# Kernel optimization log

Measured on AMD Instinct MI355X. Metric: run time of the kernel, lower is better.

## Reference

```python
import jax, jax.numpy as jnp
import numpy as np

B, CIN, COUT, H0 = 2, 256, 256, 128
GN_G = 16

def hsig(x):
    return jnp.clip(x + 3.0, 0.0, 6.0) / 6.0

def conv3x3(x, w, b):
    y = jax.lax.conv_general_dilated(x, w, (1, 1), ((1, 1), (1, 1)),
                                     dimension_numbers=('NCHW', 'OIHW', 'NCHW'))
    return y + b[None, :, None, None]

def group_norm(x, gamma, beta):
    Bn, C, H, W = x.shape
    xr = x.reshape(Bn, GN_G, C // GN_G, H, W)
    m = xr.mean((2, 3, 4), keepdims=True)
    v = xr.var((2, 3, 4), keepdims=True)
    xn = ((xr - m) * jax.lax.rsqrt(v + 1e-5)).reshape(Bn, C, H, W)
    return xn * gamma[None, :, None, None] + beta[None, :, None, None]

def mdconv(x, offset, mask, weight, stride):
    # Modulated deformable conv v2, 3x3 kernel, padding=1, zero-pad bilinear sampling.
    Bn, C, H, W = x.shape
    K2 = mask.shape[1]  # 9 kernel taps
    Ho, Wo = mask.shape[2], mask.shape[3]
    off = offset.reshape(Bn, K2, 2, Ho, Wo)  # (dy, dx) per tap (mmcv channel order)
    ki = jnp.arange(K2)
    py = (jnp.arange(Ho, dtype=x.dtype) * stride - 1.0)[None, None, :, None] \
         + (ki // 3).astype(x.dtype)[None, :, None, None] + off[:, :, 0]
    px = (jnp.arange(Wo, dtype=x.dtype) * stride - 1.0)[None, None, None, :] \
         + (ki % 3).astype(x.dtype)[None, :, None, None] + off[:, :, 1]
    y0f = jnp.floor(py); x0f = jnp.floor(px)
    wy = py - y0f; wx = px - x0f
    y0 = y0f.astype(jnp.int32); x0 = x0f.astype(jnp.int32)
    xf = x.reshape(Bn, C, H * W)

    def gather(yy, xx):
        valid = ((yy >= 0) & (yy < H) & (xx >= 0) & (xx < W)).astype(x.dtype)
        idx = jnp.clip(yy, 0, H - 1) * W + jnp.clip(xx, 0, W - 1)
        g = jax.vmap(lambda f, i: f[:, i])(xf, idx.reshape(Bn, -1))
        return g.reshape(Bn, C, K2, Ho, Wo) * valid[:, None]

    val = (gather(y0, x0) * ((1 - wy) * (1 - wx))[:, None]
           + gather(y0, x0 + 1) * ((1 - wy) * wx)[:, None]
           + gather(y0 + 1, x0) * (wy * (1 - wx))[:, None]
           + gather(y0 + 1, x0 + 1) * (wy * wx)[:, None])
    val = val * mask[:, None]
    return jnp.einsum('bckhw,ock->bohw', val, weight.reshape(weight.shape[0], C, K2))

def scale_attn(f, w, b):
    p = f.mean((2, 3))                  # global avg pool -> (B, C)
    s = hsig(jax.nn.relu(p @ w.T + b))  # (B, 1)
    return s[:, :, None, None]

def dyrelu(x, w1, b1, w2, b2):
    Bn, C = x.shape[0], x.shape[1]
    p = x.mean((2, 3))
    h = jax.nn.relu(p @ w1.T + b1)
    c = (hsig(h @ w2.T + b2) - 0.5).reshape(Bn, 4, C)  # a1, b1, a2, b2
    e = lambda t: t[:, :, None, None]
    a1 = c[:, 0] * 2.0 + 1.0
    a2 = c[:, 2] * 2.0
    return jnp.maximum(x * e(a1) + e(c[:, 1]), x * e(a2) + e(c[:, 3]))

def resize_align(x, Ho, Wo):
    # bilinear resize, align_corners=True
    Bn, C, H, W = x.shape
    sy = jnp.arange(Ho, dtype=x.dtype) * ((H - 1) / (Ho - 1))
    sx = jnp.arange(Wo, dtype=x.dtype) * ((W - 1) / (Wo - 1))
    yl = jnp.floor(sy).astype(jnp.int32); yh = jnp.minimum(yl + 1, H - 1)
    xl = jnp.floor(sx).astype(jnp.int32); xh = jnp.minimum(xl + 1, W - 1)
    wy = (sy - yl)[None, None, :, None]
    wx = (sx - xl)[None, None, None, :]
    t = x[:, :, yl, :] * (1 - wy) + x[:, :, yh, :] * wy
    return t[:, :, :, xl] * (1 - wx) + t[:, :, :, xh] * wx

def _forward(x0, x1, x2, w_off, b_off, w_mid, g_mid, be_mid, w_low, g_low, be_low,
             w_high, g_high, be_high, w_sa, b_sa, w_dy1, b_dy1, w_dy2, b_dy2):
    xs = [x0, x1, x2]
    L = len(xs)
    outs = []
    for l in range(L):
        om = conv3x3(xs[l], w_off, b_off)
        offset = om[:, :18]
        mask = jax.nn.sigmoid(om[:, 18:])
        mid = group_norm(mdconv(xs[l], offset, mask, w_mid, 1), g_mid, be_mid)
        sum_feat = mid * scale_attn(mid, w_sa, b_sa)
        n = 1
        if l > 0:
            low = group_norm(mdconv(xs[l - 1], offset, mask, w_low, 2), g_low, be_low)
            sum_feat = sum_feat + low * scale_attn(low, w_sa, b_sa)
            n += 1
        if l < L - 1:
            # x[l+1] has half resolution; subsample offset/mask to its grid
            o2 = offset[:, :, ::2, ::2]
            m2 = mask[:, :, ::2, ::2]
            high = group_norm(mdconv(xs[l + 1], o2, m2, w_high, 1), g_high, be_high)
            high = resize_align(high, xs[l].shape[2], xs[l].shape[3])
            sum_feat = sum_feat + high * scale_attn(high, w_sa, b_sa)
            n += 1
        outs.append(dyrelu(sum_feat / n, w_dy1, b_dy1, w_dy2, b_dy2))
    return tuple(outs)

def setup_inputs():
    key = jax.random.key(0)
    ks = jax.random.split(key, 20)
    f32 = jnp.float32
    rn = lambda k, s: jax.random.normal(k, s, f32)
    return {
        'x0': rn(ks[0], (B, CIN, H0, H0)),
        'x1': rn(ks[1], (B, CIN, H0 // 2, H0 // 2)),
        'x2': rn(ks[2], (B, CIN, H0 // 4, H0 // 4)),
        'w_off': 0.01 * rn(ks[3], (27, CIN, 3, 3)),
        'b_off': jnp.zeros((27,), f32),
        'w_mid': 0.05 * rn(ks[4], (COUT, CIN, 3, 3)),
        'g_mid': 1.0 + 0.1 * rn(ks[5], (COUT,)),
        'be_mid': 0.1 * rn(ks[6], (COUT,)),
        'w_low': 0.05 * rn(ks[7], (COUT, CIN, 3, 3)),
        'g_low': 1.0 + 0.1 * rn(ks[8], (COUT,)),
        'be_low': 0.1 * rn(ks[9], (COUT,)),
        'w_high': 0.05 * rn(ks[10], (COUT, CIN, 3, 3)),
        'g_high': 1.0 + 0.1 * rn(ks[11], (COUT,)),
        'be_high': 0.1 * rn(ks[12], (COUT,)),
        'w_sa': 0.05 * rn(ks[13], (1, COUT)),
        'b_sa': jnp.zeros((1,), f32),
        'w_dy1': 0.05 * rn(ks[14], (COUT // 4, COUT)),
        'b_dy1': jnp.zeros((COUT // 4,), f32),
        'w_dy2': 0.05 * rn(ks[15], (4 * COUT, COUT // 4)),
        'b_dy2': jnp.zeros((4 * COUT,), f32),
    }

def reference(x0, x1, x2, w_off, b_off, w_mid, g_mid, be_mid, w_low, g_low, be_low,
              w_high, g_high, be_high, w_sa, b_sa, w_dy1, b_dy1, w_dy2, b_dy2):
    return _forward(x0, x1, x2, w_off, b_off, w_mid, g_mid, be_mid, w_low, g_low,
                    be_low, w_high, g_high, be_high, w_sa, b_sa, w_dy1, b_dy1,
                    w_dy2, b_dy2)
```

## Files before the change

### kernel.cpp

```cpp
#include <hip/hip_runtime.h>
#include <hip/hip_bf16.h>
#include <math.h>

#define CIN 256
#define COUT 256
#define NB 2
#define GN_GROUPS 16

typedef __attribute__((ext_vector_type(8))) short short8;
typedef __attribute__((ext_vector_type(4))) float floatx4;

__device__ __forceinline__ float b2f(unsigned short u) {
  union { unsigned int i; float f; } v;
  v.i = ((unsigned int)u) << 16;
  return v.f;
}
__device__ __forceinline__ unsigned short f2b(float f) {
  union { float f; unsigned int i; } v;
  v.f = f;
  unsigned int r = (v.i + 0x7FFFu + ((v.i >> 16) & 1u)) >> 16;
  return (unsigned short)r;
}
__device__ __forceinline__ float lo2f(unsigned int u) {
  union { unsigned int i; float f; } v;
  v.i = u << 16;
  return v.f;
}
__device__ __forceinline__ float hi2f(unsigned int u) {
  union { unsigned int i; float f; } v;
  v.i = u & 0xffff0000u;
  return v.f;
}
__device__ __forceinline__ unsigned int pk2(float a, float b) {
  union { __hip_bfloat162 h; unsigned int u; } v;
  v.h = __float22bfloat162_rn(float2{a, b});
  return v.u;
}

struct SetB {
  const float *x0, *x1, *x2, *wm, *wl, *wh, *wof;
  unsigned short *t0, *t1, *t2, *l0, *l1, *l2;
  unsigned short *wtm, *wtl, *wth, *wo;
  float* stats;
};

__global__ __launch_bounds__(256) void setup_kernel(SetB A) {
  __shared__ float tile[64][65];
  int bx = blockIdx.x, t = threadIdx.x;
  if (bx < 2688) {
    int xg = bx % 336;
    int rem = bx / 336;
    int yg = rem & 3, zg = rem >> 2;
    int li = (xg >= 256 ? 1 : 0) + (xg >= 320 ? 1 : 0);
    int local = xg - (li == 0 ? 0 : (li == 1 ? 256 : 320));
    const float* x = li == 0 ? A.x0 : (li == 1 ? A.x1 : A.x2);
    unsigned short* xT = li == 0 ? A.t0 : (li == 1 ? A.t1 : A.t2);
    unsigned short* xLo = li == 0 ? A.l0 : (li == 1 ? A.l1 : A.l2);
    int P = li == 0 ? 16384 : (li == 1 ? 4096 : 1024);
    int pBase = local * 64, cBase = yg * 64, b = zg;
    int pl = t & 63, ch = t >> 6;
    const float* xb = x + ((size_t)b * CIN + cBase) * P + pBase;
#pragma unroll
    for (int e = 0; e < 16; e++) {
      int c = ch * 16 + e;
      tile[c][pl] = xb[(size_t)c * P + pl];
    }
    __syncthreads();
    size_t obase = ((size_t)b * P + pBase) * CIN + cBase;
    int cl = t & 63, pr = t >> 6;
#pragma unroll
    for (int e = 0; e < 16; e++) {
      int p = pr * 16 + e;
      float v = tile[cl][p];
      unsigned short h = f2b(v);
      xT[obase + (size_t)p * CIN + cl] = h;
      xLo[obase + (size_t)p * CIN + cl] = f2b(v - b2f(h));
    }
  } else if (bx < 9600) {
    int lb = bx - 2688;
    int sel = (lb >= 2304 ? 1 : 0) + (lb >= 4608 ? 1 : 0);
    const float* w = sel == 0 ? A.wm : (sel == 1 ? A.wl : A.wh);
    unsigned short* wt = sel == 0 ? A.wtm : (sel == 1 ? A.wtl : A.wth);
    int idx = (lb - sel * 2304) * 256 + t;
    int e = idx & 7;
    int lane = (idx >> 3) & 63;
    int i = (idx >> 9) & 3;
    int wv = (idx >> 11) & 3;
    int kc = idx >> 13;
    int oc = wv * 64 + i * 16 + (lane & 15);
    int c = (kc & 7) * 32 + (lane >> 4) * 8 + e;
    int tap = kc >> 3;
    wt[idx] = f2b(w[(size_t)oc * 2304 + c * 9 + tap]);
  } else if (bx < 10176) {
    int idx = (bx - 9600) * 256 + t;
    int sel = idx / 73728;
    int r = idx % 73728;
    int k = r / 8192;
    int r2 = r % 8192;
    int cbk = r2 / 1024;
    int oc = (r2 / 32) % 32;
    int ch = r2 % 32;
    int c = cbk * 32 + ch;
    float val = (oc < 27) ? A.wof[(size_t)oc * 2304 + c * 9 + k] : 0.0f;
    float hi = b2f(f2b(val));
    A.wo[idx] = sel ? f2b(val - hi) : f2b(val);
  } else {
    int idx = (bx - 10176) * 256 + t;
    if (idx < 10752) A.stats[idx] = 0.f;
  }
}

struct CoL {
  const unsigned short* xhi;
  const unsigned short* xlo;
  float* om;
  int H, W, Cs, cshift, Rs, P;
};
struct CoB { CoL L[3]; int off[4]; };

__global__ __launch_bounds__(256) void conv_offset_kernel(
    CoB B, const unsigned short* __restrict__ wo,
    const float* __restrict__ bias) {
  __shared__ unsigned short s_hi[204 * 40];
  __shared__ unsigned short s_lo[204 * 40];
  int bx = blockIdx.x;
  int li = (bx >= B.off[1] ? 1 : 0) + (bx >= B.off[2] ? 1 : 0);
  CoL L = B.L[li];
  int local = bx - B.off[li];
  int tpb = L.P / 64;
  int b = local / tpb, pxt = local % tpb;
  int t = threadIdx.x;
  int pbase = pxt * 64;
  int r0 = pbase / L.W;
  int c0 = pbase % L.W;
  int Ct = L.Cs + 2;
  int Npos = Ct * (L.Rs + 2);
  const unsigned short* xhib = L.xhi + (size_t)b * L.P * CIN;
  const unsigned short* xlob = L.xlo + (size_t)b * L.P * CIN;

  int lane = t & 63, wv = t >> 6, quad = lane >> 4, ln = lane & 15;
  int pl = wv * 16 + ln;
  int pi_ = pl >> L.cshift;
  int pj_ = pl & (L.Cs - 1);

  floatx4 acc0 = {0.f, 0.f, 0.f, 0.f}, acc1 = {0.f, 0.f, 0.f, 0.f};

  for (int cb = 0; cb < 8; cb++) {
    __syncthreads();
    for (int e = t; e < Npos * 4; e += 256) {
      int pos = e >> 2, oct = e & 3;
      int r = pos / Ct, c = pos % Ct;
      int gy = r0 - 1 + r, gx = c0 - 1 + c;
      uint4 vhi = {0, 0, 0, 0}, vlo = {0, 0, 0, 0};
      if (gy >= 0 && gy < L.H && gx >= 0 && gx < L.W) {
        size_t off = ((size_t)(gy * L.W + gx)) * CIN + cb * 32 + oct * 8;
        vhi = *(const uint4*)(xhib + off);
        vlo = *(const uint4*)(xlob + off);
      }
      *(uint4*)&s_hi[pos * 40 + oct * 8] = vhi;
      *(uint4*)&s_lo[pos * 40 + oct * 8] = vlo;
    }
    __syncthreads();
#pragma unroll
    for (int tap = 0; tap < 9; tap++) {
      int dy = tap / 3 - 1, dx = tap % 3 - 1;
      const unsigned short* wb0 = wo + (size_t)((0 * 9 + tap) * 8 + cb) * 1024;
      const unsigned short* wb1 = wo + (size_t)((1 * 9 + tap) * 8 + cb) * 1024;
      short8 whi0 = *(const short8*)(wb0 + ln * 32 + quad * 8);
      short8 whi1 = *(const short8*)(wb0 + (16 + ln) * 32 + quad * 8);
      short8 wlo0 = *(const short8*)(wb1 + ln * 32 + quad * 8);
      short8 wlo1 = *(const short8*)(wb1 + (16 + ln) * 32 + quad * 8);
      int pos = (pi_ + dy + 1) * Ct + (pj_ + dx + 1);
      short8 bhi = *(const short8*)&s_hi[pos * 40 + quad * 8];
      short8 blo = *(const short8*)&s_lo[pos * 40 + quad * 8];
      acc0 = __builtin_amdgcn_mfma_f32_16x16x32_bf16(whi0, bhi, acc0, 0, 0, 0);
      acc1 = __builtin_amdgcn_mfma_f32_16x16x32_bf16(whi1, bhi, acc1, 0, 0, 0);
      acc0 = __builtin_amdgcn_mfma_f32_16x16x32_bf16(wlo0, bhi, acc0, 0, 0, 0);
      acc1 = __builtin_amdgcn_mfma_f32_16x16x32_bf16(wlo1, bhi, acc1, 0, 0, 0);
      acc0 = __builtin_amdgcn_mfma_f32_16x16x32_bf16(whi0, blo, acc0, 0, 0, 0);
      acc1 = __builtin_amdgcn_mfma_f32_16x16x32_bf16(whi1, blo, acc1, 0, 0, 0);
    }
  }

  int px = pbase + pl;
#pragma unroll
  for (int i2 = 0; i2 < 2; i2++) {
#pragma unroll
    for (int r = 0; r < 4; r++) {
      int oc = i2 * 16 + quad * 4 + r;
      if (oc < 27) {
        float val = (i2 == 0 ? acc0[r] : acc1[r]) + bias[oc];
        if (oc >= 18) val = 1.f / (1.f + __expf(-val));
        L.om[((size_t)b * 27 + oc) * L.P + px] = val;
      }
    }
  }
}

struct MdP {
  const unsigned short* xT;
  const unsigned short* wt;
  float* outf;
  const float* om;
  float* sum;
  float* sumsq;
  float* wsum;
  int Hi, Wi, Wo, lWo, stride, omStep, omW, omP, ltile, Hro;
};
struct MdBatch { MdP p[7]; int off[7]; };

#define GATHER(k, G)                                                        \
  do {                                                                      \
    int tap_ = (k) >> 3, cbk_ = (k) & 7;                                    \
    int yy_ = s_yy[tap_][gpx], xx_ = s_xx[tap_][gpx];                       \
    int y0_ = yy_ & 0xffff, y1_ = (yy_ >> 16) & 0xffff;                     \
    int x0_ = xx_ & 0xffff, x1_ = (xx_ >> 16) & 0xffff;                     \
    const unsigned short* gb_ = xTb + cbk_ * 32 + goct * 8;                 \
    G[0] = *(const uint4*)(gb_ + (size_t)(y0_ + x0_) * CIN);                \
    G[1] = *(const uint4*)(gb_ + (size_t)(y0_ + x1_) * CIN);                \
    G[2] = *(const uint4*)(gb_ + (size_t)(y1_ + x0_) * CIN);                \
    G[3] = *(const uint4*)(gb_ + (size_t)(y1_ + x1_) * CIN);                \
  } while (0)

#define PACKC(k, G)                                                         \
  do {                                                                      \
    float4 cw_ = s_cw[(k) >> 3][gpx];                                       \
    float r_[8];                                                            \
    _Pragma("unroll") for (int j_ = 0; j_ < 4; j_++) {                      \
      unsigned int a_ = ((unsigned int*)&G[0])[j_];                         \
      unsigned int b2_ = ((unsigned int*)&G[1])[j_];                        \
      unsigned int c_ = ((unsigned int*)&G[2])[j_];                         \
      unsigned int d_ = ((unsigned int*)&G[3])[j_];                         \
      r_[2 * j_] = cw_.x * lo2f(a_) + cw_.y * lo2f(b2_) +                   \
                   cw_.z * lo2f(c_) + cw_.w * lo2f(d_);                     \
      r_[2 * j_ + 1] = cw_.x * hi2f(a_) + cw_.y * hi2f(b2_) +               \
                       cw_.z * hi2f(c_) + cw_.w * hi2f(d_);                 \
    }                                                                       \
    uint4 pk_;                                                              \
    pk_.x = pk2(r_[0], r_[1]);                                              \
    pk_.y = pk2(r_[2], r_[3]);                                              \
    pk_.z = pk2(r_[4], r_[5]);                                              \
    pk_.w = pk2(r_[6], r_[7]);                                              \
    *(uint4*)&s_col[(k) & 3][gpx][goct * 8] = pk_;                          \
  } while (0)

#define LOADAF(k, AF)                                                       \
  do {                                                                      \
    const short8* wp_ = (const short8*)(P.wt) +                             \
                        ((size_t)((k) * 16 + wv * 4) << 6) + lane;          \
    _Pragma("unroll") for (int i_ = 0; i_ < 4; i_++) AF[i_] = wp_[i_ * 64]; \
  } while (0)

#define MFMA16(AF, CUR)                                                     \
  do {                                                                      \
    short8 bfr_[4];                                                         \
    _Pragma("unroll") for (int j_ = 0; j_ < 4; j_++)                        \
      bfr_[j_] = *(const short8*)&s_col[CUR][j_ * 16 + ln][quad * 8];       \
    _Pragma("unroll") for (int i_ = 0; i_ < 4; i_++)                        \
      _Pragma("unroll") for (int j_ = 0; j_ < 4; j_++)                      \
        acc[i_][j_] = __builtin_amdgcn_mfma_f32_16x16x32_bf16(              \
            AF[i_], bfr_[j_], acc[i_][j_], 0, 0, 0);                        \
  } while (0)

#define PHASE_BAR()                                                         \
  do {                                                                      \
    asm volatile("s_waitcnt lgkmcnt(0)" ::: "memory");                      \
    __builtin_amdgcn_s_barrier();                                           \
    __builtin_amdgcn_sched_barrier(0);                                      \
  } while (0)

__global__ __launch_bounds__(256, 3) void mdconv_kernel(MdBatch B) {
  __shared__ float4 s_cw[9][64];
  __shared__ int s_yy[9][64];
  __shared__ int s_xx[9][64];
  __shared__ unsigned short s_col[4][64][40];
  __shared__ float s_prof[64];

  int bx = blockIdx.x;
  int pidx = 0;
#pragma unroll
  for (int i = 1; i < 7; i++) pidx += (bx >= B.off[i]) ? 1 : 0;
  MdP P = B.p[pidx];
  int local = bx - B.off[pidx];
  int ntile = 1 << P.ltile;
  int nslots = (NB << P.ltile) >> 3;
  int flat = (local & 7) * nslots + (local >> 3);
  int b = flat >> P.ltile;
  int pxt = flat & (ntile - 1);
  int Po = P.Wo << P.lWo;
  const unsigned short* xTb = P.xT + (size_t)b * P.Hi * P.Wi * CIN;

  int t = threadIdx.x;
  if (P.wsum) {
    if (t < P.Wo) s_prof[t] = 0.f;
    __syncthreads();
    if (t < P.Hro) {
      float r = (float)(P.Wo - 1) / (float)(P.Hro - 1);
      float sy = (float)t * r;
      int yl = (int)floorf(sy);
      float fy = sy - (float)yl;
      int yh = min(yl + 1, P.Wo - 1);
      atomicAdd(&s_prof[yl], 1.f - fy);
      atomicAdd(&s_prof[yh], fy);
    }
  }
  for (int e = t; e < 576; e += 256) {
    int k = e / 64, px = e % 64;
    int p = pxt * 64 + px;
    int i = p >> P.lWo, j = p & (P.Wo - 1);
    int pc = (i * P.omStep) * P.omW + j * P.omStep;
    const float* omb = P.om + (size_t)b * 27 * P.omP;
    float offy = omb[(size_t)(2 * k) * P.omP + pc];
    float offx = omb[(size_t)(2 * k + 1) * P.omP + pc];
    float m = omb[(size_t)(18 + k) * P.omP + pc];
    float py = (float)(i * P.stride) - 1.0f + (float)(k / 3) + offy;
    float pxf = (float)(j * P.stride) - 1.0f + (float)(k % 3) + offx;
    float y0f = floorf(py), x0f = floorf(pxf);
    float wy = py - y0f, wx = pxf - x0f;
    int y0 = (int)y0f, x0 = (int)x0f;
    int y1 = y0 + 1, x1 = x0 + 1;
    float vy0 = (y0 >= 0 && y0 < P.Hi) ? 1.f : 0.f;
    float vy1 = (y1 >= 0 && y1 < P.Hi) ? 1.f : 0.f;
    float vx0 = (x0 >= 0 && x0 < P.Wi) ? 1.f : 0.f;
    float vx1 = (x1 >= 0 && x1 < P.Wi) ? 1.f : 0.f;
    float4 cw;
    cw.x = (1.f - wy) * (1.f - wx) * m * vy0 * vx0;
    cw.y = (1.f - wy) * wx * m * vy0 * vx1;
    cw.z = wy * (1.f - wx) * m * vy1 * vx0;
    cw.w = wy * wx * m * vy1 * vx1;
    s_cw[k][px] = cw;
    int y0c = min(max(y0, 0), P.Hi - 1), y1c = min(max(y1, 0), P.Hi - 1);
    int x0c = min(max(x0, 0), P.Wi - 1), x1c = min(max(x1, 0), P.Wi - 1);
    s_yy[k][px] = (y0c * P.Wi) | ((y1c * P.Wi) << 16);
    s_xx[k][px] = x0c | (x1c << 16);
  }
  __syncthreads();

  floatx4 acc[4][4];
#pragma unroll
  for (int i = 0; i < 4; i++)
#pragma unroll
    for (int j = 0; j < 4; j++) acc[i][j] = (floatx4){0.f, 0.f, 0.f, 0.f};

  int lane = t & 63, wv = t >> 6;
  int quad = lane >> 4, ln = lane & 15;
  int wOc = wv * 64;
  int gpx = t >> 2, goct = t & 3;

  uint4 gA[4], gB[4];
  short8 afA[4], afB[4];

  GATHER(0, gA);
  GATHER(1, gB);
  PACKC(0, gA);
  PACKC(1, gB);
  GATHER(2, gA);
  GATHER(3, gB);
  LOADAF(0, afA);
  LOADAF(1, afB);
  PHASE_BAR();

  for (int c0 = 0; c0 < 72; c0 += 2) {
    MFMA16(afA, c0 & 3);
    if (c0 + 2 < 72) {
      LOADAF(c0 + 2, afA);
      PACKC(c0 + 2, gA);
    }
    if (c0 + 4 < 72) GATHER(c0 + 4, gA);
    MFMA16(afB, (c0 + 1) & 3);
    if (c0 + 3 < 72) {
      LOADAF(c0 + 3, afB);
      PACKC(c0 + 3, gB);
    }
    if (c0 + 5 < 72) GATHER(c0 + 5, gB);
    PHASE_BAR();
  }

#pragma unroll
  for (int i = 0; i < 4; i++) {
    int ocB = wOc + i * 16 + quad * 4;
#pragma unroll
    for (int j = 0; j < 4; j++) {
      int px = pxt * 64 + j * 16 + ln;
#pragma unroll
      for (int r = 0; r < 4; r++)
        P.outf[((size_t)b * COUT + ocB + r) * Po + px] = acc[i][j][r];
    }
  }

  float pw[4];
  if (P.wsum) {
#pragma unroll
    for (int j = 0; j < 4; j++) {
      int px = pxt * 64 + j * 16 + ln;
      pw[j] = s_prof[px >> P.lWo] * s_prof[px & (P.Wo - 1)];
    }
  }
#pragma unroll
  for (int i = 0; i < 4; i++) {
    int ocB = wOc + i * 16 + quad * 4;
#pragma unroll
    for (int r = 0; r < 4; r++) {
      float s1 = 0.f, s2 = 0.f, sw = 0.f;
#pragma unroll
      for (int j = 0; j < 4; j++) {
        float v = acc[i][j][r];
        s1 += v;
        s2 += v * v;
        if (P.wsum) sw += v * pw[j];
      }
#pragma unroll
      for (int m = 1; m < 16; m <<= 1) {
        s1 += __shfl_xor(s1, m, 64);
        s2 += __shfl_xor(s2, m, 64);
        if (P.wsum) sw += __shfl_xor(sw, m, 64);
      }
      if (ln == 0) {
        atomicAdd(&P.sum[b * COUT + ocB + r], s1);
        atomicAdd(&P.sumsq[b * COUT + ocB + r], s2);
        if (P.wsum) atomicAdd(&P.wsum[b * COUT + ocB + r], sw);
      }
    }
  }
}

struct PrepL {
  const float* st;
  float *Am, *Bm, *Al, *Bl, *Ah, *Bh, *svec, *coef;
  float invP, invPh, invn;
  int hasLow, hasHigh;
};
struct PrepB { PrepL L[3]; };

__global__ __launch_bounds__(256) void prep_all_kernel(
    PrepB PB, const float* __restrict__ g_mid, const float* __restrict__ be_mid,
    const float* __restrict__ g_low, const float* __restrict__ be_low,
    const float* __restrict__ g_high, const float* __restrict__ be_high,
    const float* __restrict__ w_sa, const float* __restrict__ b_sa,
    const float* __restrict__ w1, const float* __restrict__ b1,
    const float* __restrict__ w2, const float* __restrict__ b2) {
  __shared__ float s_m[3][NB][GN_GROUPS], s_iv[3][NB][GN_GROUPS];
  __shared__ float s_mean[3][NB][COUT];
  __shared__ float s_s[3][NB];
  __shared__ float s_nm[NB][COUT];
  __shared__ float s_h[NB][64];
  PrepL L = PB.L[blockIdx.x];
  const float* sumM = L.st;
  const float* sqM = L.st + 512;
  const float* sumL = L.st + 1024;
  const float* sqL = L.st + 1536;
  const float* sumH = L.st + 2048;
  const float* sqH = L.st + 2560;
  const float* swsum = L.st + 3072;
  int hasLow = L.hasLow, hasHigh = L.hasHigh;
  float invP = L.invP, invPh = L.invPh, invn = L.invn;
  int tid = threadIdx.x;

  if (tid < 96) {
    int path = tid / 32, b = (tid >> 4) & 1, g = tid & 15;
    int active = (path == 0) || (path == 1 && hasLow) || (path == 2 && hasHigh);
    if (active) {
      const float* su = path == 0 ? sumM : (path == 1 ? sumL : sumH);
      const float* sq = path == 0 ? sqM : (path == 1 ? sqL : sqH);
      float invN = ((path == 2) ? invPh : invP) * (1.f / 16.f);
      float s = 0.f, q = 0.f;
      for (int c = g * 16; c < g * 16 + 16; c++) {
        s += su[b * COUT + c];
        q += sq[b * COUT + c];
      }
      float m = s * invN;
      float v = q * invN - m * m;
      s_m[path][b][g] = m;
      s_iv[path][b][g] = rsqrtf(v + 1e-5f);
    }
  }
  __syncthreads();
  for (int idx = tid; idx < 3 * NB * COUT; idx += 256) {
    int path = idx / (NB * COUT);
    int r = idx % (NB * COUT);
    int b = r / COUT, c = r % COUT, g = c >> 4;
    int active = (path == 0) || (path == 1 && hasLow) || (path == 2 && hasHigh);
    if (active) {
      const float* ga = path == 0 ? g_mid : (path == 1 ? g_low : g_high);
      const float* be = path == 0 ? be_mid : (path == 1 ? be_low : be_high);
      float a = ga[c] * s_iv[path][b][g];
      float bb = be[c] - s_m[path][b][g] * a;
      float mean;
      if (path == 2)
        mean = a * (swsum[r] * invP) + bb;
      else {
        const float* su = path == 0 ? sumM : sumL;
        mean = a * (su[r] * invP) + bb;
      }
      float* Ad = path == 0 ? L.Am : (path == 1 ? L.Al : L.Ah);
      float* Bd = path == 0 ? L.Bm : (path == 1 ? L.Bl : L.Bh);
      Ad[r] = a;
      Bd[r] = bb;
      s_mean[path][b][c] = mean;
    }
  }
  __syncthreads();
  if (tid < 6) {
    int path = tid >> 1, b = tid & 1;
    int active = (path == 0) || (path == 1 && hasLow) || (path == 2 && hasHigh);
    float s = 0.f;
    if (active) {
      float t = 0.f;
      for (int c = 0; c < COUT; c++) t += s_mean[path][b][c] * w_sa[c];
      t += b_sa[0];
      t = fmaxf(t, 0.0f);
      s = fminf(fmaxf(t + 3.f, 0.f), 6.f) * (1.f / 6.f);
      L.svec[path * NB + b] = s;
    }
    s_s[path][b] = s;
  }
  __syncthreads();
  for (int idx = tid; idx < NB * COUT; idx += 256) {
    int b = idx / COUT, c = idx % COUT;
    float v = s_s[0][b] * s_mean[0][b][c];
    if (hasLow) v += s_s[1][b] * s_mean[1][b][c];
    if (hasHigh) v += s_s[2][b] * s_mean[2][b][c];
    s_nm[b][c] = v * invn;
  }
  __syncthreads();
  if (tid < NB * 64) {
    int b = tid / 64, j = tid % 64;
    float t = b1[j];
    for (int c = 0; c < COUT; c++) t += s_nm[b][c] * w1[j * COUT + c];
    s_h[b][j] = fmaxf(t, 0.f);
  }
  __syncthreads();
  for (int idx = tid; idx < NB * 1024; idx += 256) {
    int b = idx / 1024, i = idx % 1024;
    float t = b2[i];
    for (int j = 0; j < 64; j++) t += s_h[b][j] * w2[i * 64 + j];
    L.coef[idx] = fminf(fmaxf(t + 3.f, 0.f), 6.f) * (1.f / 6.f) - 0.5f;
  }
}

struct ApL {
  const float* featM; const float* featL; const float* featH;
  const float* Am; const float* Bm; const float* Al; const float* Bl;
  const float* Ah; const float* Bh; const float* svec; const float* coef;
  float* out;
  int lP, lHo, Hh, hasLow, hasHigh;
  float invn;
};
struct ApB { ApL L[3]; int off[4]; };

__global__ __launch_bounds__(256) void fused_apply_kernel(ApB A) {
  int bx = blockIdx.x;
  int li = (bx >= A.off[1] ? 1 : 0) + (bx >= A.off[2] ? 1 : 0);
  ApL L = A.L[li];
  int idx = (bx - A.off[li]) * 256 + threadIdx.x;
  int bc = idx >> L.lP;
  int p = idx & ((1 << L.lP) - 1);
  int b = bc >> 8, c = bc & 255;
  float v = (L.featM[idx] * L.Am[bc] + L.Bm[bc]) * L.svec[b];
  if (L.hasLow) v += (L.featL[idx] * L.Al[bc] + L.Bl[bc]) * L.svec[2 + b];
  if (L.hasHigh) {
    int Ho = 1 << L.lHo;
    int Y = p >> L.lHo, X = p & (Ho - 1);
    float r = (float)(L.Hh - 1) / (float)(Ho - 1);
    float sy = (float)Y * r, sx = (float)X * r;
    int yl = (int)floorf(sy), xl = (int)floorf(sx);
    int yh = min(yl + 1, L.Hh - 1), xh = min(xl + 1, L.Hh - 1);
    float wy = sy - (float)yl, wx = sx - (float)xl;
    const float* fp = L.featH + (size_t)bc * L.Hh * L.Hh;
    float t0 = fp[yl * L.Hh + xl] * (1.f - wx) + fp[yl * L.Hh + xh] * wx;
    float t1 = fp[yh * L.Hh + xl] * (1.f - wx) + fp[yh * L.Hh + xh] * wx;
    v += ((t0 * (1.f - wy) + t1 * wy) * L.Ah[bc] + L.Bh[bc]) * L.svec[4 + b];
  }
  float xv = v * L.invn;
  float a1 = L.coef[b * 1024 + c] * 2.f + 1.f;
  float b1v = L.coef[b * 1024 + 256 + c];
  float a2 = L.coef[b * 1024 + 512 + c] * 2.f;
  float b2v = L.coef[b * 1024 + 768 + c];
  L.out[idx] = fmaxf(xv * a1 + b1v, xv * a2 + b2v);
}

extern "C" void kernel_launch(void* const* d_in, const int* in_sizes, int n_in,
                              void* d_out, int out_size, void* d_ws,
                              size_t ws_size, hipStream_t stream) {
  (void)in_sizes; (void)n_in; (void)out_size; (void)ws_size;
  const float* x[3] = {(const float*)d_in[0], (const float*)d_in[1],
                       (const float*)d_in[2]};
  const float* w_off = (const float*)d_in[3];
  const float* b_off = (const float*)d_in[4];
  const float* w_mid = (const float*)d_in[5];
  const float* g_mid = (const float*)d_in[6];
  const float* be_mid = (const float*)d_in[7];
  const float* w_low = (const float*)d_in[8];
  const float* g_low = (const float*)d_in[9];
  const float* be_low = (const float*)d_in[10];
  const float* w_high = (const float*)d_in[11];
  const float* g_high = (const float*)d_in[12];
  const float* be_high = (const float*)d_in[13];
  const float* w_sa = (const float*)d_in[14];
  const float* b_sa = (const float*)d_in[15];
  const float* w_dy1 = (const float*)d_in[16];
  const float* b_dy1 = (const float*)d_in[17];
  const float* w_dy2 = (const float*)d_in[18];
  const float* b_dy2 = (const float*)d_in[19];

  float* out = (float*)d_out;
  char* wsb = (char*)d_ws;
  size_t o = 0;
  unsigned short* xT0 = (unsigned short*)(wsb + o); o += 16777216;
  unsigned short* xT1 = (unsigned short*)(wsb + o); o += 4194304;
  unsigned short* xT2 = (unsigned short*)(wsb + o); o += 1048576;
  unsigned short* wtm = (unsigned short*)(wsb + o); o += 1179648;
  unsigned short* wtl = (unsigned short*)(wsb + o); o += 1179648;
  unsigned short* wth = (unsigned short*)(wsb + o); o += 1179648;
  unsigned short* wo  = (unsigned short*)(wsb + o); o += 294912;
  float* om0 = (float*)(wsb + o); o += 3538944;
  float* om1 = (float*)(wsb + o); o += 884736;
  float* om2 = (float*)(wsb + o); o += 221184;
  float* arena = (float*)(wsb + o); o += 65011712;
  float* stats = (float*)(wsb + o); o += 43072;
  float* Am = (float*)(wsb + o); o += 6144;
  float* Bm = (float*)(wsb + o); o += 6144;
  float* Al = (float*)(wsb + o); o += 6144;
  float* Bl = (float*)(wsb + o); o += 6144;
  float* Ah = (float*)(wsb + o); o += 6144;
  float* Bh = (float*)(wsb + o); o += 6144;
  float* svec = (float*)(wsb + o); o += 192;
  float* dycoef = (float*)(wsb + o); o += 24576;

  float* featM0 = arena;
  float* featH0 = arena + 8388608;
  float* featM1 = arena + 10485760;
  float* featL1 = arena + 12582912;
  float* featH1 = arena + 14680064;
  float* featM2 = arena + 15204352;
  float* featL2 = arena + 15728640;

  unsigned short* xLo0 = (unsigned short*)arena;
  unsigned short* xLo1 = xLo0 + 8388608;
  unsigned short* xLo2 = xLo1 + 2097152;

  SetB sb = {x[0], x[1], x[2], w_mid, w_low, w_high, w_off,
             xT0, xT1, xT2, xLo0, xLo1, xLo2, wtm, wtl, wth, wo, stats};
  setup_kernel<<<10219, 256, 0, stream>>>(sb);

  CoB cob;
  cob.L[0] = {xT0, xLo0, om0, 128, 128, 64, 6, 1, 16384};
  cob.L[1] = {xT1, xLo1, om1, 64, 64, 64, 6, 1, 4096};
  cob.L[2] = {xT2, xLo2, om2, 32, 32, 32, 5, 2, 1024};
  cob.off[0] = 0; cob.off[1] = 512; cob.off[2] = 640; cob.off[3] = 672;
  conv_offset_kernel<<<672, 256, 0, stream>>>(cob, wo, b_off);

  float* S0 = stats;
  float* S1 = stats + 3584;
  float* S2 = stats + 7168;
  MdBatch mb;
  mb.p[0] = {xT0, wtm, featM0, om0, S0, S0 + 512, nullptr,
             128, 128, 128, 7, 1, 1, 128, 16384, 8, 0};
  mb.p[1] = {xT1, wth, featH0, om0, S0 + 2048, S0 + 2560, S0 + 3072,
             64, 64, 64, 6, 1, 2, 128, 16384, 6, 128};
  mb.p[2] = {xT1, wtm, featM1, om1, S1, S1 + 512, nullptr,
             64, 64, 64, 6, 1, 1, 64, 4096, 6, 0};
  mb.p[3] = {xT0, wtl, featL1, om1, S1 + 1024, S1 + 1536, nullptr,
             128, 128, 64, 6, 2, 1, 64, 4096, 6, 0};
  mb.p[4] = {xT2, wth, featH1, om1, S1 + 2048, S1 + 2560, S1 + 3072,
             32, 32, 32, 5, 1, 2, 64, 4096, 4, 64};
  mb.p[5] = {xT2, wtm, featM2, om2, S2, S2 + 512, nullptr,
             32, 32, 32, 5, 1, 1, 32, 1024, 4, 0};
  mb.p[6] = {xT1, wtl, featL2, om2, S2 + 1024, S2 + 1536, nullptr,
             64, 64, 32, 5, 2, 1, 32, 1024, 4, 0};
  mb.off[0] = 0;   mb.off[1] = 512; mb.off[2] = 640; mb.off[3] = 768;
  mb.off[4] = 896; mb.off[5] = 928; mb.off[6] = 960;
  mdconv_kernel<<<992, 256, 0, stream>>>(mb);

  PrepB pb;
  {
    const int Hs[3] = {128, 64, 32};
    const float nterm[3] = {2.f, 3.f, 2.f};
    for (int l = 0; l < 3; l++) {
      int H = Hs[l];
      int Pp = H * H;
      int Ph = (H / 2) * (H / 2);
      pb.L[l] = {stats + l * 3584, Am + l * 512, Bm + l * 512, Al + l * 512,
                 Bl + l * 512, Ah + l * 512, Bh + l * 512, svec + l * 16,
                 dycoef + l * 2048, 1.0f / (float)Pp, 1.0f / (float)Ph,
                 1.0f / nterm[l], l > 0 ? 1 : 0, l < 2 ? 1 : 0};
    }
  }
  prep_all_kernel<<<3, 256, 0, stream>>>(pb, g_mid, be_mid, g_low, be_low,
                                         g_high, be_high, w_sa, b_sa, w_dy1,
                                         b_dy1, w_dy2, b_dy2);

  ApB ab;
  ab.L[0] = {featM0, featM0, featH0, Am, Bm, Al, Bl, Ah, Bh, svec, dycoef,
             out, 14, 7, 64, 0, 1, 0.5f};
  ab.L[1] = {featM1, featL1, featH1, Am + 512, Bm + 512, Al + 512, Bl + 512,
             Ah + 512, Bh + 512, svec + 16, dycoef + 2048, out + 8388608,
             12, 6, 32, 1, 1, 1.0f / 3.0f};
  ab.L[2] = {featM2, featL2, featM2, Am + 1024, Bm + 1024, Al + 1024,
             Bl + 1024, Ah + 1024, Bh + 1024, svec + 32, dycoef + 4096,
             out + 10485760, 10, 5, 16, 1, 0, 0.5f};
  ab.off[0] = 0; ab.off[1] = 32768; ab.off[2] = 40960; ab.off[3] = 43008;
  fused_apply_kernel<<<43008, 256, 0, stream>>>(ab);
}
```

Before: 411.4 us.

## Double mdconv pixel tile to 128 and vectorize fused apply by four

The deformable-conv kernel now processes 128 output pixels per block instead of 64. Each thread gathers and packs two pixels, and each wave issues 4x8 MFMA tiles, so every loaded weight fragment is reused across twice as many columns, with the grid halved to 496 blocks. Occupancy drops to 2 blocks per CU because the accumulators, gather registers and LDS footprint all double. Separately, the fused apply kernel handles four contiguous pixels per thread with float4 loads and stores, cutting its grid by four and sharing the per-channel coefficients and row interpolation setup.

```diff
diff --git a/kernel.cpp b/kernel.cpp
--- a/kernel.cpp
+++ b/kernel.cpp
@@ -209,28 +209,28 @@
 };
 struct MdBatch { MdP p[7]; int off[7]; };
 
-#define GATHER(k, G)                                                        \
+#define GATHER1(k, Gp, PX)                                                  \
   do {                                                                      \
     int tap_ = (k) >> 3, cbk_ = (k) & 7;                                    \
-    int yy_ = s_yy[tap_][gpx], xx_ = s_xx[tap_][gpx];                       \
+    int yy_ = s_yy[tap_][PX], xx_ = s_xx[tap_][PX];                         \
     int y0_ = yy_ & 0xffff, y1_ = (yy_ >> 16) & 0xffff;                     \
     int x0_ = xx_ & 0xffff, x1_ = (xx_ >> 16) & 0xffff;                     \
     const unsigned short* gb_ = xTb + cbk_ * 32 + goct * 8;                 \
-    G[0] = *(const uint4*)(gb_ + (size_t)(y0_ + x0_) * CIN);                \
-    G[1] = *(const uint4*)(gb_ + (size_t)(y0_ + x1_) * CIN);                \
-    G[2] = *(const uint4*)(gb_ + (size_t)(y1_ + x0_) * CIN);                \
-    G[3] = *(const uint4*)(gb_ + (size_t)(y1_ + x1_) * CIN);                \
+    (Gp)[0] = *(const uint4*)(gb_ + (size_t)(y0_ + x0_) * CIN);             \
+    (Gp)[1] = *(const uint4*)(gb_ + (size_t)(y0_ + x1_) * CIN);             \
+    (Gp)[2] = *(const uint4*)(gb_ + (size_t)(y1_ + x0_) * CIN);             \
+    (Gp)[3] = *(const uint4*)(gb_ + (size_t)(y1_ + x1_) * CIN);             \
   } while (0)
 
-#define PACKC(k, G)                                                         \
+#define PACK1(k, Gp, PX)                                                    \
   do {                                                                      \
-    float4 cw_ = s_cw[(k) >> 3][gpx];                                       \
+    float4 cw_ = s_cw[(k) >> 3][PX];                                        \
     float r_[8];                                                            \
     _Pragma("unroll") for (int j_ = 0; j_ < 4; j_++) {                      \
-      unsigned int a_ = ((unsigned int*)&G[0])[j_];                         \
-      unsigned int b2_ = ((unsigned int*)&G[1])[j_];                        \
-      unsigned int c_ = ((unsigned int*)&G[2])[j_];                         \
-      unsigned int d_ = ((unsigned int*)&G[3])[j_];                         \
+      unsigned int a_ = ((unsigned int*)&(Gp)[0])[j_];                      \
+      unsigned int b2_ = ((unsigned int*)&(Gp)[1])[j_];                     \
+      unsigned int c_ = ((unsigned int*)&(Gp)[2])[j_];                      \
+      unsigned int d_ = ((unsigned int*)&(Gp)[3])[j_];                      \
       r_[2 * j_] = cw_.x * lo2f(a_) + cw_.y * lo2f(b2_) +                   \
                    cw_.z * lo2f(c_) + cw_.w * lo2f(d_);                     \
       r_[2 * j_ + 1] = cw_.x * hi2f(a_) + cw_.y * hi2f(b2_) +               \
@@ -241,7 +241,19 @@
     pk_.y = pk2(r_[2], r_[3]);                                              \
     pk_.z = pk2(r_[4], r_[5]);                                              \
     pk_.w = pk2(r_[6], r_[7]);                                              \
-    *(uint4*)&s_col[(k) & 3][gpx][goct * 8] = pk_;                          \
+    *(uint4*)&s_col[(k) & 3][PX][goct * 8] = pk_;                           \
+  } while (0)
+
+#define GATHER(k, G)                                                        \
+  do {                                                                      \
+    GATHER1(k, &(G)[0], gpx0);                                              \
+    GATHER1(k, &(G)[4], gpx1);                                              \
+  } while (0)
+
+#define PACKC(k, G)                                                         \
+  do {                                                                      \
+    PACK1(k, &(G)[0], gpx0);                                                \
+    PACK1(k, &(G)[4], gpx1);                                                \
   } while (0)
 
 #define LOADAF(k, AF)                                                       \
@@ -251,13 +263,13 @@
     _Pragma("unroll") for (int i_ = 0; i_ < 4; i_++) AF[i_] = wp_[i_ * 64]; \
   } while (0)
 
-#define MFMA16(AF, CUR)                                                     \
+#define MFMA32(AF, CUR)                                                     \
   do {                                                                      \
-    short8 bfr_[4];                                                         \
-    _Pragma("unroll") for (int j_ = 0; j_ < 4; j_++)                        \
+    short8 bfr_[8];                                                         \
+    _Pragma("unroll") for (int j_ = 0; j_ < 8; j_++)                        \
       bfr_[j_] = *(const short8*)&s_col[CUR][j_ * 16 + ln][quad * 8];       \
     _Pragma("unroll") for (int i_ = 0; i_ < 4; i_++)                        \
-      _Pragma("unroll") for (int j_ = 0; j_ < 4; j_++)                      \
+      _Pragma("unroll") for (int j_ = 0; j_ < 8; j_++)                      \
         acc[i_][j_] = __builtin_amdgcn_mfma_f32_16x16x32_bf16(              \
             AF[i_], bfr_[j_], acc[i_][j_], 0, 0, 0);                        \
   } while (0)
@@ -269,12 +281,12 @@
     __builtin_amdgcn_sched_barrier(0);                                      \
   } while (0)
 
-__global__ __launch_bounds__(256, 3) void mdconv_kernel(MdBatch B) {
-  __shared__ float4 s_cw[9][64];
-  __shared__ int s_yy[9][64];
-  __shared__ int s_xx[9][64];
-  __shared__ unsigned short s_col[4][64][40];
-  __shared__ float s_prof[64];
+__global__ __launch_bounds__(256, 2) void mdconv_kernel(MdBatch B) {
+  __shared__ float4 s_cw[9][128];
+  __shared__ int s_yy[9][128];
+  __shared__ int s_xx[9][128];
+  __shared__ unsigned short s_col[4][128][40];
+  __shared__ float s_prof[128];
 
   int bx = blockIdx.x;
   int pidx = 0;
@@ -304,9 +316,9 @@
       atomicAdd(&s_prof[yh], fy);
     }
   }
-  for (int e = t; e < 576; e += 256) {
-    int k = e / 64, px = e % 64;
-    int p = pxt * 64 + px;
+  for (int e = t; e < 1152; e += 256) {
+    int k = e >> 7, px = e & 127;
+    int p = pxt * 128 + px;
     int i = p >> P.lWo, j = p & (P.Wo - 1);
     int pc = (i * P.omStep) * P.omW + j * P.omStep;
     const float* omb = P.om + (size_t)b * 27 * P.omP;
@@ -336,18 +348,19 @@
   }
   __syncthreads();
 
-  floatx4 acc[4][4];
+  floatx4 acc[4][8];
 #pragma unroll
   for (int i = 0; i < 4; i++)
 #pragma unroll
-    for (int j = 0; j < 4; j++) acc[i][j] = (floatx4){0.f, 0.f, 0.f, 0.f};
+    for (int j = 0; j < 8; j++) acc[i][j] = (floatx4){0.f, 0.f, 0.f, 0.f};
 
   int lane = t & 63, wv = t >> 6;
   int quad = lane >> 4, ln = lane & 15;
   int wOc = wv * 64;
-  int gpx = t >> 2, goct = t & 3;
-
-  uint4 gA[4], gB[4];
+  int gpx0 = t >> 2, gpx1 = (t >> 2) + 64;
+  int goct = t & 3;
+
+  uint4 gA[8], gB[8];
   short8 afA[4], afB[4];
 
   GATHER(0, gA);
@@ -361,13 +374,13 @@
   PHASE_BAR();
 
   for (int c0 = 0; c0 < 72; c0 += 2) {
-    MFMA16(afA, c0 & 3);
+    MFMA32(afA, c0 & 3);
     if (c0 + 2 < 72) {
       LOADAF(c0 + 2, afA);
       PACKC(c0 + 2, gA);
     }
     if (c0 + 4 < 72) GATHER(c0 + 4, gA);
-    MFMA16(afB, (c0 + 1) & 3);
+    MFMA32(afB, (c0 + 1) & 3);
     if (c0 + 3 < 72) {
       LOADAF(c0 + 3, afB);
       PACKC(c0 + 3, gB);
@@ -380,19 +393,19 @@
   for (int i = 0; i < 4; i++) {
     int ocB = wOc + i * 16 + quad * 4;
 #pragma unroll
-    for (int j = 0; j < 4; j++) {
-      int px = pxt * 64 + j * 16 + ln;
+    for (int j = 0; j < 8; j++) {
+      int px = pxt * 128 + j * 16 + ln;
 #pragma unroll
       for (int r = 0; r < 4; r++)
         P.outf[((size_t)b * COUT + ocB + r) * Po + px] = acc[i][j][r];
     }
   }
 
-  float pw[4];
+  float pw[8];
   if (P.wsum) {
 #pragma unroll
-    for (int j = 0; j < 4; j++) {
-      int px = pxt * 64 + j * 16 + ln;
+    for (int j = 0; j < 8; j++) {
+      int px = pxt * 128 + j * 16 + ln;
       pw[j] = s_prof[px >> P.lWo] * s_prof[px & (P.Wo - 1)];
     }
   }
@@ -403,7 +416,7 @@
     for (int r = 0; r < 4; r++) {
       float s1 = 0.f, s2 = 0.f, sw = 0.f;
 #pragma unroll
-      for (int j = 0; j < 4; j++) {
+      for (int j = 0; j < 8; j++) {
         float v = acc[i][j][r];
         s1 += v;
         s2 += v * v;
@@ -552,31 +565,60 @@
   int bx = blockIdx.x;
   int li = (bx >= A.off[1] ? 1 : 0) + (bx >= A.off[2] ? 1 : 0);
   ApL L = A.L[li];
-  int idx = (bx - A.off[li]) * 256 + threadIdx.x;
+  int idx = ((bx - A.off[li]) * 256 + threadIdx.x) * 4;
   int bc = idx >> L.lP;
-  int p = idx & ((1 << L.lP) - 1);
+  int p0 = idx & ((1 << L.lP) - 1);
   int b = bc >> 8, c = bc & 255;
-  float v = (L.featM[idx] * L.Am[bc] + L.Bm[bc]) * L.svec[b];
-  if (L.hasLow) v += (L.featL[idx] * L.Al[bc] + L.Bl[bc]) * L.svec[2 + b];
+  float am = L.Am[bc], bm = L.Bm[bc], sm = L.svec[b];
+  float4 fm = *(const float4*)&L.featM[idx];
+  float v0 = (fm.x * am + bm) * sm;
+  float v1 = (fm.y * am + bm) * sm;
+  float v2 = (fm.z * am + bm) * sm;
+  float v3 = (fm.w * am + bm) * sm;
+  if (L.hasLow) {
+    float al = L.Al[bc], bl = L.Bl[bc], sl = L.svec[2 + b];
+    float4 fl = *(const float4*)&L.featL[idx];
+    v0 += (fl.x * al + bl) * sl;
+    v1 += (fl.y * al + bl) * sl;
+    v2 += (fl.z * al + bl) * sl;
+    v3 += (fl.w * al + bl) * sl;
+  }
   if (L.hasHigh) {
     int Ho = 1 << L.lHo;
-    int Y = p >> L.lHo, X = p & (Ho - 1);
+    int Y = p0 >> L.lHo, X0 = p0 & (Ho - 1);
     float r = (float)(L.Hh - 1) / (float)(Ho - 1);
-    float sy = (float)Y * r, sx = (float)X * r;
-    int yl = (int)floorf(sy), xl = (int)floorf(sx);
-    int yh = min(yl + 1, L.Hh - 1), xh = min(xl + 1, L.Hh - 1);
-    float wy = sy - (float)yl, wx = sx - (float)xl;
+    float sy = (float)Y * r;
+    int yl = (int)floorf(sy);
+    int yh = min(yl + 1, L.Hh - 1);
+    float wy = sy - (float)yl;
+    float ah = L.Ah[bc], bh = L.Bh[bc], sh = L.svec[4 + b];
     const float* fp = L.featH + (size_t)bc * L.Hh * L.Hh;
-    float t0 = fp[yl * L.Hh + xl] * (1.f - wx) + fp[yl * L.Hh + xh] * wx;
-    float t1 = fp[yh * L.Hh + xl] * (1.f - wx) + fp[yh * L.Hh + xh] * wx;
-    v += ((t0 * (1.f - wy) + t1 * wy) * L.Ah[bc] + L.Bh[bc]) * L.svec[4 + b];
-  }
-  float xv = v * L.invn;
+    const float* fpl = fp + yl * L.Hh;
+    const float* fph = fp + yh * L.Hh;
+    float hv[4];
+#pragma unroll
+    for (int j = 0; j < 4; j++) {
+      float sx = (float)(X0 + j) * r;
+      int xl = (int)floorf(sx);
+      int xh = min(xl + 1, L.Hh - 1);
+      float wx = sx - (float)xl;
+      float t0 = fpl[xl] * (1.f - wx) + fpl[xh] * wx;
+      float t1 = fph[xl] * (1.f - wx) + fph[xh] * wx;
+      hv[j] = ((t0 * (1.f - wy) + t1 * wy) * ah + bh) * sh;
+    }
+    v0 += hv[0]; v1 += hv[1]; v2 += hv[2]; v3 += hv[3];
+  }
   float a1 = L.coef[b * 1024 + c] * 2.f + 1.f;
   float b1v = L.coef[b * 1024 + 256 + c];
   float a2 = L.coef[b * 1024 + 512 + c] * 2.f;
   float b2v = L.coef[b * 1024 + 768 + c];
-  L.out[idx] = fmaxf(xv * a1 + b1v, xv * a2 + b2v);
+  float4 o;
+  float x0 = v0 * L.invn, x1 = v1 * L.invn, x2 = v2 * L.invn, x3 = v3 * L.invn;
+  o.x = fmaxf(x0 * a1 + b1v, x0 * a2 + b2v);
+  o.y = fmaxf(x1 * a1 + b1v, x1 * a2 + b2v);
+  o.z = fmaxf(x2 * a1 + b1v, x2 * a2 + b2v);
+  o.w = fmaxf(x3 * a1 + b1v, x3 * a2 + b2v);
+  *(float4*)&L.out[idx] = o;
 }
 
 extern "C" void kernel_launch(void* const* d_in, const int* in_sizes, int n_in,
@@ -655,22 +697,22 @@
   float* S2 = stats + 7168;
   MdBatch mb;
   mb.p[0] = {xT0, wtm, featM0, om0, S0, S0 + 512, nullptr,
-             128, 128, 128, 7, 1, 1, 128, 16384, 8, 0};
+             128, 128, 128, 7, 1, 1, 128, 16384, 7, 0};
   mb.p[1] = {xT1, wth, featH0, om0, S0 + 2048, S0 + 2560, S0 + 3072,
-             64, 64, 64, 6, 1, 2, 128, 16384, 6, 128};
+             64, 64, 64, 6, 1, 2, 128, 16384, 5, 128};
   mb.p[2] = {xT1, wtm, featM1, om1, S1, S1 + 512, nullptr,
-             64, 64, 64, 6, 1, 1, 64, 4096, 6, 0};
+             64, 64, 64, 6, 1, 1, 64, 4096, 5, 0};
   mb.p[3] = {xT0, wtl, featL1, om1, S1 + 1024, S1 + 1536, nullptr,
-             128, 128, 64, 6, 2, 1, 64, 4096, 6, 0};
+             128, 128, 64, 6, 2, 1, 64, 4096, 5, 0};
   mb.p[4] = {xT2, wth, featH1, om1, S1 + 2048, S1 + 2560, S1 + 3072,
-             32, 32, 32, 5, 1, 2, 64, 4096, 4, 64};
+             32, 32, 32, 5, 1, 2, 64, 4096, 3, 64};
   mb.p[5] = {xT2, wtm, featM2, om2, S2, S2 + 512, nullptr,
-             32, 32, 32, 5, 1, 1, 32, 1024, 4, 0};
+             32, 32, 32, 5, 1, 1, 32, 1024, 3, 0};
   mb.p[6] = {xT1, wtl, featL2, om2, S2 + 1024, S2 + 1536, nullptr,
-             64, 64, 32, 5, 2, 1, 32, 1024, 4, 0};
-  mb.off[0] = 0;   mb.off[1] = 512; mb.off[2] = 640; mb.off[3] = 768;
-  mb.off[4] = 896; mb.off[5] = 928; mb.off[6] = 960;
-  mdconv_kernel<<<992, 256, 0, stream>>>(mb);
+             64, 64, 32, 5, 2, 1, 32, 1024, 3, 0};
+  mb.off[0] = 0;   mb.off[1] = 256; mb.off[2] = 320; mb.off[3] = 384;
+  mb.off[4] = 448; mb.off[5] = 464; mb.off[6] = 480;
+  mdconv_kernel<<<496, 256, 0, stream>>>(mb);
 
   PrepB pb;
   {
@@ -699,6 +741,6 @@
   ab.L[2] = {featM2, featL2, featM2, Am + 1024, Bm + 1024, Al + 1024,
              Bl + 1024, Ah + 1024, Bh + 1024, svec + 32, dycoef + 4096,
              out + 10485760, 10, 5, 16, 1, 0, 0.5f};
-  ab.off[0] = 0; ab.off[1] = 32768; ab.off[2] = 40960; ab.off[3] = 43008;
-  fused_apply_kernel<<<43008, 256, 0, stream>>>(ab);
-}
+  ab.off[0] = 0; ab.off[1] = 8192; ab.off[2] = 10240; ab.off[3] = 10752;
+  fused_apply_kernel<<<10752, 256, 0, stream>>>(ab);
+}
```

Measured after the change: 446.8 us. +8.6%, slower.
